# Kernel tuning notes

Hardware: AMD Instinct MI355X
Metric: run time of the kernel (lower is better)

Reference implementation:

```python
import jax, jax.numpy as jnp
import numpy as np

BATCH, SEQ, IN, HID, OUT = 64, 512, 512, 1024, 512


def setup_inputs() -> dict:
    key = jax.random.key(0)
    ks = jax.random.split(key, 7)
    s_ih = 1.0 / np.sqrt(IN)
    s_hh = 1.0 / np.sqrt(HID)
    return {
        "x_sequence": jax.random.normal(ks[0], (BATCH, SEQ, IN), dtype=jnp.float32),
        "W_ih": jax.random.uniform(ks[1], (HID, IN), jnp.float32, -s_ih, s_ih),
        "b_ih": jax.random.uniform(ks[2], (HID,), jnp.float32, -s_ih, s_ih),
        "W_hh": jax.random.uniform(ks[3], (HID, HID), jnp.float32, -s_hh, s_hh),
        "b_hh": jax.random.uniform(ks[4], (HID,), jnp.float32, -s_hh, s_hh),
        "W_ho": jax.random.uniform(ks[5], (OUT, HID), jnp.float32, -s_hh, s_hh),
        "b_ho": jax.random.uniform(ks[6], (OUT,), jnp.float32, -s_hh, s_hh),
    }


def reference(x_sequence, W_ih, b_ih, W_hh, b_hh, W_ho, b_ho):
    # Elman RNN: h_t = tanh(x_t @ W_ih^T + b_ih + h_{t-1} @ W_hh^T + b_hh)
    # Returned output is the projection of the FINAL hidden state only
    # (per-step outputs in the original are detached bookkeeping).
    # Precompute all input projections in one big GEMM: [B,S,H]
    x_proj = jnp.einsum("bsi,hi->bsh", x_sequence, W_ih) + b_ih + b_hh

    def step(h, xp_t):
        h_new = jnp.tanh(xp_t + h @ W_hh.T)
        return h_new, None

    h0 = jnp.zeros((x_sequence.shape[0], W_hh.shape[0]), dtype=x_sequence.dtype)
    h_final, _ = jax.lax.scan(step, h0, jnp.swapaxes(x_proj, 0, 1))  # scan over time
    output = h_final @ W_ho.T + b_ho  # [B, OUT]
    return output
```

## Files before the change

### kernel.cpp

```cpp
#include <hip/hip_runtime.h>
#include <cstdint>
#include <cstddef>

typedef unsigned short ushort_t;
typedef unsigned int uint_t;
typedef unsigned long long u64_t;
typedef __attribute__((ext_vector_type(8))) short frag16;
typedef __attribute__((ext_vector_type(8))) unsigned short u16x8;
typedef __attribute__((ext_vector_type(4))) float f32x4;

#define SEQ   512
#define INF   512
#define HID   1024
#define OUTF  512
#define GROUPS 16
#define BPG    16
#define NB     4
#define RPB    64
#define SPIN_LIMIT (1 << 18)

__device__ __forceinline__ float b2f(ushort_t u) {
    union { unsigned int i; float f; } v; v.i = ((unsigned int)u) << 16; return v.f;
}
__device__ __forceinline__ ushort_t f2b(float f) {
    unsigned int u = __float_as_uint(f);
    unsigned int r = (u + 0x7fffu + ((u >> 16) & 1u)) >> 16;
    return (ushort_t)r;
}
__device__ __forceinline__ float fast_tanh(float s) {
    const float e = __expf(2.0f * s);
    return 1.0f - 2.0f * __builtin_amdgcn_rcpf(e + 1.0f);
}

__device__ __forceinline__ void cvt8_hilo(const float* __restrict__ src, u16x8* hi, u16x8* lo) {
    const float4 x0 = *(const float4*)src;
    const float4 x1 = *(const float4*)(src + 4);
    float xs[8] = {x0.x,x0.y,x0.z,x0.w,x1.x,x1.y,x1.z,x1.w};
    u16x8 h, l;
#pragma unroll
    for (int j = 0; j < 8; ++j) {
        const ushort_t hb = f2b(xs[j]);
        h[j] = hb;
        l[j] = f2b(xs[j] - b2f(hb));
    }
    *hi = h; if (lo) *lo = l;
}
__device__ __forceinline__ u16x8 cvt8_hi(const float* __restrict__ src) {
    const float4 x0 = *(const float4*)src;
    const float4 x1 = *(const float4*)(src + 4);
    float xs[8] = {x0.x,x0.y,x0.z,x0.w,x1.x,x1.y,x1.z,x1.w};
    u16x8 h;
#pragma unroll
    for (int j = 0; j < 8; ++j) h[j] = f2b(xs[j]);
    return h;
}

__global__ __launch_bounds__(256, 2)
void xproj_kernel(const float* __restrict__ X, const float* __restrict__ Wih,
                  const float* __restrict__ bih, const float* __restrict__ bhh,
                  float* __restrict__ XP)
{
    __shared__ ushort_t Ah[128][40];
    __shared__ ushort_t Al[128][40];
    __shared__ ushort_t Bs[128][40];
    const int tid = (int)threadIdx.x;
    const int m0 = (int)blockIdx.x * 128;
    const int n0 = (int)blockIdx.y * 128;
    const int w  = tid >> 6, l = tid & 63;
    const int wm = (w & 1) * 64, wn = (w >> 1) * 64;
    const int lm = l & 15, lg = l >> 4, hk = lg * 8;
    const int sr = tid >> 2, sc = (tid & 3) * 8;

    f32x4 acc[4][4];
#pragma unroll
    for (int a = 0; a < 4; ++a)
#pragma unroll
        for (int b = 0; b < 4; ++b) { acc[a][b][0]=0.f; acc[a][b][1]=0.f; acc[a][b][2]=0.f; acc[a][b][3]=0.f; }

    for (int ko = 0; ko < INF; ko += 32) {
        __syncthreads();
        u16x8 h, lo;
        cvt8_hilo(&X[(size_t)(m0+sr)*INF + ko + sc], &h, &lo);
        *(u16x8*)&Ah[sr][sc] = h;  *(u16x8*)&Al[sr][sc] = lo;
        cvt8_hilo(&X[(size_t)(m0+sr+64)*INF + ko + sc], &h, &lo);
        *(u16x8*)&Ah[sr+64][sc] = h;  *(u16x8*)&Al[sr+64][sc] = lo;
        *(u16x8*)&Bs[sr][sc]    = cvt8_hi(&Wih[(size_t)(n0+sr)*INF + ko + sc]);
        *(u16x8*)&Bs[sr+64][sc] = cvt8_hi(&Wih[(size_t)(n0+sr+64)*INF + ko + sc]);
        __syncthreads();
        frag16 afh[4], afl[4], bf[4];
#pragma unroll
        for (int i = 0; i < 4; ++i) afh[i] = *(const frag16*)&Ah[wm + i*16 + lm][hk];
#pragma unroll
        for (int i = 0; i < 4; ++i) afl[i] = *(const frag16*)&Al[wm + i*16 + lm][hk];
#pragma unroll
        for (int i = 0; i < 4; ++i) bf[i]  = *(const frag16*)&Bs[wn + i*16 + lm][hk];
#pragma unroll
        for (int a = 0; a < 4; ++a)
#pragma unroll
            for (int b = 0; b < 4; ++b) {
                acc[a][b] = __builtin_amdgcn_mfma_f32_16x16x32_bf16(afh[a], bf[b], acc[a][b], 0, 0, 0);
                acc[a][b] = __builtin_amdgcn_mfma_f32_16x16x32_bf16(afl[a], bf[b], acc[a][b], 0, 0, 0);
            }
    }

#pragma unroll
    for (int b = 0; b < 4; ++b) {
        const int n = n0 + wn + b*16 + lm;
        const float bias = bih[n] + bhh[n];
#pragma unroll
        for (int a = 0; a < 4; ++a)
#pragma unroll
            for (int q = 0; q < 4; ++q) {
                const int m = m0 + wm + a*16 + lg*4 + q;
                XP[(size_t)m * HID + n] = acc[a][b][q] + bias;
            }
    }
}

__global__ __launch_bounds__(256, 1)
void rnn_scan_kernel(const float* __restrict__ XP, const float* __restrict__ Whh,
                     u64_t* __restrict__ Hbuf)
{
    __shared__ ushort_t Ws[RPB][1032];
    __shared__ uint_t   Hst[NB][1028];
    __shared__ float    Cred[4][4][4][16];

    const int tid = (int)threadIdx.x;
    const int w = tid >> 6, l = tid & 63;
    const int lm = l & 15, lg = l >> 4;
    const int gid = (int)blockIdx.x >> 4;
    const int r   = (int)blockIdx.x & 15;
    const int b0 = gid * NB;
    const int j0 = r * RPB;

    {
        const int rr = tid >> 2, cq = (tid & 3) * 256;
        const float* src = Whh + (size_t)(j0 + rr) * HID + cq;
#pragma unroll
        for (int i = 0; i < 32; ++i)
            *(u16x8*)&Ws[rr][cq + i*8] = cvt8_hi(&src[i*8]);
    }
    __syncthreads();

    for (int t = 0; t < SEQ; ++t) {
        float xpv[4];
        if (l < 16) {
#pragma unroll
            for (int q = 0; q < 4; ++q)
                xpv[q] = XP[(size_t)((b0 + q) * SEQ + t) * HID + (j0 + w*16 + l)];
        }

        if (t > 0) {
            {
                const u64_t* rowp = Hbuf + ((size_t)((t - 1) & 1) * 64 + b0 + w) * 1024 + l;
                const uint_t want = (uint_t)t;
                u64_t v[16];
#pragma unroll
                for (int j = 0; j < 16; ++j)
                    v[j] = __hip_atomic_load(&rowp[j*64], __ATOMIC_RELAXED,
                                             __HIP_MEMORY_SCOPE_AGENT);
                int spin = 0;
                for (;;) {
                    int bad = 0;
#pragma unroll
                    for (int j = 0; j < 16; ++j) bad |= ((uint_t)v[j] != want);
                    if (!__any(bad)) break;
                    if (++spin > SPIN_LIMIT) break;
                    __builtin_amdgcn_s_sleep(1);
#pragma unroll
                    for (int j = 0; j < 16; ++j)
                        if ((uint_t)v[j] != want)
                            v[j] = __hip_atomic_load(&rowp[j*64], __ATOMIC_RELAXED,
                                                     __HIP_MEMORY_SCOPE_AGENT);
                }
#pragma unroll
                for (int j = 0; j < 16; ++j)
                    Hst[w][l + 64*j] = (uint_t)(v[j] >> 32);
            }
            __syncthreads();

            f32x4 acc[4];
#pragma unroll
            for (int i = 0; i < 4; ++i) { acc[i][0]=0.f; acc[i][1]=0.f; acc[i][2]=0.f; acc[i][3]=0.f; }
            const int kbase = w * 256;
#pragma unroll
            for (int kk = 0; kk < 256; kk += 32) {
                const int k0 = kbase + kk;
                frag16 ahi, alo;
#pragma unroll
                for (int j = 0; j < 8; ++j) { ahi[j] = 0; alo[j] = 0; }
                if (lm < NB) {
                    const uint_t* hr = &Hst[lm][k0 + lg*8];
                    const uint4 d0 = *(const uint4*)hr;
                    const uint4 d1 = *(const uint4*)(hr + 4);
                    uint_t dd[8] = {d0.x,d0.y,d0.z,d0.w,d1.x,d1.y,d1.z,d1.w};
#pragma unroll
                    for (int j = 0; j < 8; ++j) {
                        ahi[j] = (short)(dd[j] & 0xffffu);
                        alo[j] = (short)(dd[j] >> 16);
                    }
                }
#pragma unroll
                for (int tl = 0; tl < 4; ++tl) {
                    const frag16 wf = *(const frag16*)&Ws[tl*16 + lm][k0 + lg*8];
                    acc[tl] = __builtin_amdgcn_mfma_f32_16x16x32_bf16(ahi, wf, acc[tl], 0, 0, 0);
                    acc[tl] = __builtin_amdgcn_mfma_f32_16x16x32_bf16(alo, wf, acc[tl], 0, 0, 0);
                }
            }
            if (lg == 0) {
#pragma unroll
                for (int tl = 0; tl < 4; ++tl)
#pragma unroll
                    for (int q = 0; q < 4; ++q)
                        Cred[w][tl][q][lm] = acc[tl][q];
            }
            __syncthreads();
        }

        if (l < 16) {
            const int jt = j0 + w*16 + l;
            u64_t* outp = Hbuf + ((size_t)(t & 1) * 64 + b0) * 1024 + jt;
#pragma unroll
            for (int q = 0; q < 4; ++q) {
                float s = 0.f;
                if (t > 0)
                    s = Cred[0][w][q][l] + Cred[1][w][q][l]
                      + Cred[2][w][q][l] + Cred[3][w][q][l];
                const float v = fast_tanh(s + xpv[q]);
                const ushort_t hi = f2b(v);
                const ushort_t lo = f2b(v - b2f(hi));
                const u64_t pk = ((u64_t)((uint_t)hi | ((uint_t)lo << 16)) << 32)
                               | (u64_t)(uint_t)(t + 1);
                __hip_atomic_store(&outp[(size_t)q * 1024], pk,
                                   __ATOMIC_RELAXED, __HIP_MEMORY_SCOPE_AGENT);
            }
        }
    }
}

__global__ __launch_bounds__(256)
void outproj_kernel(const u64_t* __restrict__ Hp, const float* __restrict__ Who,
                    const float* __restrict__ bho, float* __restrict__ Out)
{
    const int tid = (int)threadIdx.x;
    const int w = tid >> 6, l = tid & 63;
    const int lm = l & 15, lg = l >> 4, hk = lg * 8;
    const int n0 = (int)blockIdx.x * 64;

    f32x4 acc[4];
#pragma unroll
    for (int i = 0; i < 4; ++i) { acc[i][0]=0.f; acc[i][1]=0.f; acc[i][2]=0.f; acc[i][3]=0.f; }

    for (int k0 = 0; k0 < HID; k0 += 32) {
        const u64_t* hr = Hp + (size_t)(w*16 + lm) * HID + k0 + hk;
        frag16 ahi, alo;
#pragma unroll
        for (int j = 0; j < 8; ++j) {
            const uint_t d = (uint_t)(hr[j] >> 32);
            ahi[j] = (short)(d & 0xffffu);
            alo[j] = (short)(d >> 16);
        }
#pragma unroll
        for (int bi = 0; bi < 4; ++bi) {
            const u16x8 bv = cvt8_hi(&Who[(size_t)(n0 + bi*16 + lm) * HID + k0 + hk]);
            acc[bi] = __builtin_amdgcn_mfma_f32_16x16x32_bf16(ahi, (frag16)bv, acc[bi], 0, 0, 0);
            acc[bi] = __builtin_amdgcn_mfma_f32_16x16x32_bf16(alo, (frag16)bv, acc[bi], 0, 0, 0);
        }
    }
#pragma unroll
    for (int bi = 0; bi < 4; ++bi) {
        const int n = n0 + bi*16 + lm;
        const float bias = bho[n];
#pragma unroll
        for (int q = 0; q < 4; ++q) {
            const int b = w*16 + lg*4 + q;
            Out[(size_t)b * OUTF + n] = acc[bi][q] + bias;
        }
    }
}

extern "C" void kernel_launch(void* const* d_in, const int* in_sizes, int n_in,
                              void* d_out, int out_size, void* d_ws, size_t ws_size,
                              hipStream_t stream)
{
    const float* X   = (const float*)d_in[0];
    const float* Wih = (const float*)d_in[1];
    const float* bih = (const float*)d_in[2];
    const float* Whh = (const float*)d_in[3];
    const float* bhh = (const float*)d_in[4];
    const float* Who = (const float*)d_in[5];
    const float* bho = (const float*)d_in[6];
    float* Out = (float*)d_out;

    char* ws = (char*)d_ws;
    float* XP = (float*)ws;
    u64_t* Hbuf = (u64_t*)(ws + (size_t)32768 * 1024 * 4);

    xproj_kernel<<<dim3(256, 8), dim3(256), 0, stream>>>(X, Wih, bih, bhh, XP);

    rnn_scan_kernel<<<dim3(GROUPS * BPG), dim3(256), 0, stream>>>(XP, Whh, Hbuf);

    outproj_kernel<<<dim3(OUTF / 64), dim3(256), 0, stream>>>(Hbuf + (size_t)64 * 1024,
                                                              Who, bho, Out);
}
```

Measured before the change: 2.129 ms.

## Split recurrent matvec by output tile per wave, dropping cross-wave LDS reduction

Each wave now computes its own 16-row tile of W_hh over the full hidden dimension, instead of all four tiles over a quarter of K. This removes the shared-memory partial-sum reduction and one block barrier per time step. The hidden state is also stored as separate hi/lo bf16 arrays in LDS, so MFMA fragments load directly without per-element unpacking. Dropping the trailing barrier relies on the global per-step handshake to keep LDS reuse safe across steps.

```diff
diff --git a/kernel.cpp b/kernel.cpp
--- a/kernel.cpp
+++ b/kernel.cpp
@@ -122,8 +122,8 @@
                      u64_t* __restrict__ Hbuf)
 {
     __shared__ ushort_t Ws[RPB][1032];
-    __shared__ uint_t   Hst[NB][1028];
-    __shared__ float    Cred[4][4][4][16];
+    __shared__ ushort_t Hhi[NB][1040];
+    __shared__ ushort_t Hlo[NB][1040];
 
     const int tid = (int)threadIdx.x;
     const int w = tid >> 6, l = tid & 63;
@@ -150,6 +150,8 @@
                 xpv[q] = XP[(size_t)((b0 + q) * SEQ + t) * HID + (j0 + w*16 + l)];
         }
 
+        float sq[4] = {0.f, 0.f, 0.f, 0.f};
+
         if (t > 0) {
             {
                 const u64_t* rowp = Hbuf + ((size_t)((t - 1) & 1) * 64 + b0 + w) * 1024 + l;
@@ -174,47 +176,34 @@
                                                      __HIP_MEMORY_SCOPE_AGENT);
                 }
 #pragma unroll
-                for (int j = 0; j < 16; ++j)
-                    Hst[w][l + 64*j] = (uint_t)(v[j] >> 32);
+                for (int j = 0; j < 16; ++j) {
+                    const uint_t d = (uint_t)(v[j] >> 32);
+                    Hhi[w][l + 64*j] = (ushort_t)d;
+                    Hlo[w][l + 64*j] = (ushort_t)(d >> 16);
+                }
             }
             __syncthreads();
 
             f32x4 acc[4];
 #pragma unroll
             for (int i = 0; i < 4; ++i) { acc[i][0]=0.f; acc[i][1]=0.f; acc[i][2]=0.f; acc[i][3]=0.f; }
-            const int kbase = w * 256;
-#pragma unroll
-            for (int kk = 0; kk < 256; kk += 32) {
-                const int k0 = kbase + kk;
+#pragma unroll
+            for (int kk = 0; kk < 32; ++kk) {
+                const int k0 = kk * 32;
                 frag16 ahi, alo;
 #pragma unroll
                 for (int j = 0; j < 8; ++j) { ahi[j] = 0; alo[j] = 0; }
                 if (lm < NB) {
-                    const uint_t* hr = &Hst[lm][k0 + lg*8];
-                    const uint4 d0 = *(const uint4*)hr;
-                    const uint4 d1 = *(const uint4*)(hr + 4);
-                    uint_t dd[8] = {d0.x,d0.y,d0.z,d0.w,d1.x,d1.y,d1.z,d1.w};
-#pragma unroll
-                    for (int j = 0; j < 8; ++j) {
-                        ahi[j] = (short)(dd[j] & 0xffffu);
-                        alo[j] = (short)(dd[j] >> 16);
-                    }
+                    ahi = *(const frag16*)&Hhi[lm][k0 + lg*8];
+                    alo = *(const frag16*)&Hlo[lm][k0 + lg*8];
                 }
-#pragma unroll
-                for (int tl = 0; tl < 4; ++tl) {
-                    const frag16 wf = *(const frag16*)&Ws[tl*16 + lm][k0 + lg*8];
-                    acc[tl] = __builtin_amdgcn_mfma_f32_16x16x32_bf16(ahi, wf, acc[tl], 0, 0, 0);
-                    acc[tl] = __builtin_amdgcn_mfma_f32_16x16x32_bf16(alo, wf, acc[tl], 0, 0, 0);
-                }
-            }
-            if (lg == 0) {
-#pragma unroll
-                for (int tl = 0; tl < 4; ++tl)
-#pragma unroll
-                    for (int q = 0; q < 4; ++q)
-                        Cred[w][tl][q][lm] = acc[tl][q];
-            }
-            __syncthreads();
+                const frag16 wf = *(const frag16*)&Ws[w*16 + lm][k0 + lg*8];
+                acc[kk & 3] = __builtin_amdgcn_mfma_f32_16x16x32_bf16(ahi, wf, acc[kk & 3], 0, 0, 0);
+                acc[kk & 3] = __builtin_amdgcn_mfma_f32_16x16x32_bf16(alo, wf, acc[kk & 3], 0, 0, 0);
+            }
+#pragma unroll
+            for (int q = 0; q < 4; ++q)
+                sq[q] = (acc[0][q] + acc[1][q]) + (acc[2][q] + acc[3][q]);
         }
 
         if (l < 16) {
@@ -222,11 +211,7 @@
             u64_t* outp = Hbuf + ((size_t)(t & 1) * 64 + b0) * 1024 + jt;
 #pragma unroll
             for (int q = 0; q < 4; ++q) {
-                float s = 0.f;
-                if (t > 0)
-                    s = Cred[0][w][q][l] + Cred[1][w][q][l]
-                      + Cred[2][w][q][l] + Cred[3][w][q][l];
-                const float v = fast_tanh(s + xpv[q]);
+                const float v = fast_tanh(sq[q] + xpv[q]);
                 const ushort_t hi = f2b(v);
                 const ushort_t lo = f2b(v - b2f(hi));
                 const u64_t pk = ((u64_t)((uint_t)hi | ((uint_t)lo << 16)) << 32)
```

Result: slower. 2.220 ms (+4.3%).
